# Kernel optimization log

Measured on AMD Instinct MI355X. Metric: run time of the kernel, lower is better.

## Reference

```python
import jax, jax.numpy as jnp
import numpy as np


def setup_inputs() -> dict:
    key = jax.random.key(0)
    k1, k2, k3, k4 = jax.random.split(key, 4)
    Nc, Ng, C = 262144, 393216, 32
    DIM = 96  # N_VOX / 2**(N_LAYER - scale - 1) with scale=2
    return {
        "current_values": jax.random.normal(k1, (Nc, C), dtype=jnp.float32),
        "global_values": jax.random.normal(k2, (Ng, C), dtype=jnp.float32),
        "current_coords": jax.random.randint(k3, (Nc, 3), 0, DIM, dtype=jnp.int32),
        "global_coords": jax.random.randint(k4, (Ng, 3), 0, 110, dtype=jnp.int32),
        "relative_origin": jnp.zeros((3,), dtype=jnp.int32),
        "dim": DIM,
    }


def reference(current_values, global_values, current_coords, global_coords,
              relative_origin, dim):
    """GRUFusion.convert2dense (FUSION.FULL=False) + the gather of the dense
    hidden/input features at the updated (=current) coords that feeds ConvGRU.
    Returns [Nc, 2C]: concat(x_gather, h_gather)."""
    C = current_values.shape[-1]
    cc = current_coords  # [Nc,3], guaranteed in [0, dim)
    gc = global_coords - relative_origin[None, :]  # [Ng,3]

    # in-bounds mask for global coords relative to current fragment bbox
    valid = jnp.all((gc < dim) & (gc >= 0), axis=-1)  # [Ng]

    # occupancy of current coords (sparse_to_dense_torch(current_coords, 1, ...))
    occ = jnp.zeros((dim, dim, dim), jnp.int32)
    occ = occ.at[cc[:, 0], cc[:, 1], cc[:, 2]].set(1)

    # gather occupancy at (clamped-safe) global coords; refine valid mask
    gc_safe = jnp.where(valid[:, None], gc, 0)
    hit = occ[gc_safe[:, 0], gc_safe[:, 1], gc_safe[:, 2]] != 0
    valid = valid & hit

    # sparse_to_dense_channel(global_coords[valid], global_value[valid], ...):
    # route invalid rows out of bounds so the scatter drops them.
    gc_scat = jnp.where(valid[:, None], gc, dim)
    global_vol = jnp.zeros((dim, dim, dim, C), global_values.dtype)
    global_vol = global_vol.at[gc_scat[:, 0], gc_scat[:, 1], gc_scat[:, 2]].set(
        global_values, mode='drop')

    # sparse_to_dense_channel(current_coords, current_values, ...)
    current_vol = jnp.zeros((dim, dim, dim, C), current_values.dtype)
    current_vol = current_vol.at[cc[:, 0], cc[:, 1], cc[:, 2]].set(current_values)

    # updated_coords = current_coords (FUSION.FULL is False); gather GRU inputs
    h = global_vol[cc[:, 0], cc[:, 1], cc[:, 2]]   # hidden state  [Nc,C]
    x = current_vol[cc[:, 0], cc[:, 1], cc[:, 2]]  # current input [Nc,C]
    return jnp.concatenate([x, h], axis=-1)  # [Nc, 2C]
```

## Files before the change

kernel.cpp:

```cpp
#include <hip/hip_runtime.h>

#define DIMC 96
#define VOX (DIMC * DIMC * DIMC)
#define C 32

typedef float f32x4 __attribute__((ext_vector_type(4)));

__global__ void scatter_idx_both(const int* __restrict__ cc,
                                 const int* __restrict__ gc,
                                 const int* __restrict__ origin,
                                 int nc, int ng,
                                 int* __restrict__ cmap,
                                 int* __restrict__ gmap) {
    int i = blockIdx.x * blockDim.x + threadIdx.x;
    if (i < nc) {
        int x = cc[3 * i + 0];
        int y = cc[3 * i + 1];
        int z = cc[3 * i + 2];
        atomicMax(&cmap[(x * DIMC + y) * DIMC + z], i);
    } else {
        int k = i - nc;
        if (k < ng) {
            int x = gc[3 * k + 0] - origin[0];
            int y = gc[3 * k + 1] - origin[1];
            int z = gc[3 * k + 2] - origin[2];
            if ((unsigned)x < (unsigned)DIMC && (unsigned)y < (unsigned)DIMC &&
                (unsigned)z < (unsigned)DIMC) {
                atomicMax(&gmap[(x * DIMC + y) * DIMC + z], k);
            }
        }
    }
}

__global__ void gather_out_kernel(const f32x4* __restrict__ cur_vals,
                                  const f32x4* __restrict__ glob_vals,
                                  const int* __restrict__ cc,
                                  const int* __restrict__ cmap,
                                  const int* __restrict__ gmap,
                                  int nc, f32x4* __restrict__ out) {
    const int lane = threadIdx.x & 15;
    const int sub  = threadIdx.x >> 4;
    const int base = blockIdx.x * 64 + sub;
    const bool isx = lane < 8;
    const int* __restrict__ map = isx ? cmap : gmap;
    const f32x4* __restrict__ src = isx ? cur_vals : glob_vals;
    const int l = lane & 7;

    int p[4], v[4], j[4];
    f32x4 r[4];

#pragma unroll
    for (int q = 0; q < 4; ++q) p[q] = base + q * 16;

#pragma unroll
    for (int q = 0; q < 4; ++q) {
        int pp = p[q] < nc ? p[q] : 0;
        int x = cc[3 * pp + 0];
        int y = cc[3 * pp + 1];
        int z = cc[3 * pp + 2];
        v[q] = (x * DIMC + y) * DIMC + z;
    }
#pragma unroll
    for (int q = 0; q < 4; ++q) j[q] = map[v[q]];
#pragma unroll
    for (int q = 0; q < 4; ++q) {
        r[q] = (f32x4)(0.f);
        if (j[q] >= 0) r[q] = src[(size_t)j[q] * 8 + l];
    }
#pragma unroll
    for (int q = 0; q < 4; ++q) {
        if (p[q] < nc)
            __builtin_nontemporal_store(r[q], &out[(size_t)p[q] * 16 + lane]);
    }
}

extern "C" void kernel_launch(void* const* d_in, const int* in_sizes, int n_in,
                              void* d_out, int out_size, void* d_ws, size_t ws_size,
                              hipStream_t stream) {
    const f32x4* cur_vals = (const f32x4*)d_in[0];
    const f32x4* glob_vals = (const f32x4*)d_in[1];
    const int* cur_coords = (const int*)d_in[2];
    const int* glob_coords = (const int*)d_in[3];
    const int* rel_origin = (const int*)d_in[4];

    int nc = in_sizes[2] / 3;
    int ng = in_sizes[3] / 3;

    int* cmap = (int*)d_ws;
    int* gmap = cmap + VOX;

    hipMemsetAsync(d_ws, 0xFF, (size_t)2 * VOX * sizeof(int), stream);

    const int B = 256;
    int total = nc + ng;
    scatter_idx_both<<<(total + B - 1) / B, B, 0, stream>>>(
        cur_coords, glob_coords, rel_origin, nc, ng, cmap, gmap);

    int blocks = (nc + 63) / 64;
    gather_out_kernel<<<blocks, B, 0, stream>>>(
        cur_vals, glob_vals, cur_coords, cmap, gmap, nc, (f32x4*)d_out);
}
```

Baseline: 167.7 us.

## Vectorize coord loads, cache voxel ids, and double gather work per block

```diff
diff --git a/kernel.cpp b/kernel.cpp
--- a/kernel.cpp
+++ b/kernel.cpp
@@ -6,69 +6,101 @@
 
 typedef float f32x4 __attribute__((ext_vector_type(4)));
 
-__global__ void scatter_idx_both(const int* __restrict__ cc,
+__device__ __forceinline__ int voxid(int x, int y, int z) {
+    return (x * DIMC + y) * DIMC + z;
+}
+
+__global__ void scatter_idx_both(const int4* __restrict__ cc4,
+                                 const int4* __restrict__ gc4,
+                                 const int* __restrict__ cc,
                                  const int* __restrict__ gc,
                                  const int* __restrict__ origin,
                                  int nc, int ng,
                                  int* __restrict__ cmap,
-                                 int* __restrict__ gmap) {
-    int i = blockIdx.x * blockDim.x + threadIdx.x;
-    if (i < nc) {
-        int x = cc[3 * i + 0];
-        int y = cc[3 * i + 1];
-        int z = cc[3 * i + 2];
-        atomicMax(&cmap[(x * DIMC + y) * DIMC + z], i);
-    } else {
-        int k = i - nc;
-        if (k < ng) {
-            int x = gc[3 * k + 0] - origin[0];
-            int y = gc[3 * k + 1] - origin[1];
-            int z = gc[3 * k + 2] - origin[2];
+                                 int* __restrict__ gmap,
+                                 int* __restrict__ cvox) {
+    const int nq_c = nc >> 2, nq_g = ng >> 2;
+    int t = blockIdx.x * blockDim.x + threadIdx.x;
+
+    if (t < nq_c) {
+        int4 a = cc4[3 * t], b = cc4[3 * t + 1], c = cc4[3 * t + 2];
+        int i = 4 * t;
+        int v0 = voxid(a.x, a.y, a.z);
+        int v1 = voxid(a.w, b.x, b.y);
+        int v2 = voxid(b.z, b.w, c.x);
+        int v3 = voxid(c.y, c.z, c.w);
+        atomicMax(&cmap[v0], i);
+        atomicMax(&cmap[v1], i + 1);
+        atomicMax(&cmap[v2], i + 2);
+        atomicMax(&cmap[v3], i + 3);
+        *reinterpret_cast<int4*>(cvox + i) = make_int4(v0, v1, v2, v3);
+    } else if (t - nq_c < nq_g) {
+        int k4 = t - nq_c;
+        int4 a = gc4[3 * k4], b = gc4[3 * k4 + 1], c = gc4[3 * k4 + 2];
+        int ox = origin[0], oy = origin[1], oz = origin[2];
+        int k = 4 * k4;
+        int xs[4] = {a.x - ox, a.w - ox, b.z - ox, c.y - ox};
+        int ys[4] = {a.y - oy, b.x - oy, b.w - oy, c.z - oy};
+        int zs[4] = {a.z - oz, b.y - oz, c.x - oz, c.w - oz};
+#pragma unroll
+        for (int q = 0; q < 4; ++q) {
+            if ((unsigned)xs[q] < (unsigned)DIMC &&
+                (unsigned)ys[q] < (unsigned)DIMC &&
+                (unsigned)zs[q] < (unsigned)DIMC) {
+                atomicMax(&gmap[voxid(xs[q], ys[q], zs[q])], k + q);
+            }
+        }
+    } else if (t == nq_c + nq_g) {
+        for (int i = nq_c * 4; i < nc; ++i) {
+            int v = voxid(cc[3 * i], cc[3 * i + 1], cc[3 * i + 2]);
+            atomicMax(&cmap[v], i);
+            cvox[i] = v;
+        }
+    } else if (t == nq_c + nq_g + 1) {
+        int ox = origin[0], oy = origin[1], oz = origin[2];
+        for (int k = nq_g * 4; k < ng; ++k) {
+            int x = gc[3 * k] - ox, y = gc[3 * k + 1] - oy, z = gc[3 * k + 2] - oz;
             if ((unsigned)x < (unsigned)DIMC && (unsigned)y < (unsigned)DIMC &&
-                (unsigned)z < (unsigned)DIMC) {
-                atomicMax(&gmap[(x * DIMC + y) * DIMC + z], k);
-            }
+                (unsigned)z < (unsigned)DIMC)
+                atomicMax(&gmap[voxid(x, y, z)], k);
         }
     }
 }
 
-__global__ void gather_out_kernel(const f32x4* __restrict__ cur_vals,
-                                  const f32x4* __restrict__ glob_vals,
-                                  const int* __restrict__ cc,
-                                  const int* __restrict__ cmap,
-                                  const int* __restrict__ gmap,
-                                  int nc, f32x4* __restrict__ out) {
+__global__ __launch_bounds__(256) void gather_out_kernel(
+    const f32x4* __restrict__ cur_vals,
+    const f32x4* __restrict__ glob_vals,
+    const int* __restrict__ cvox,
+    const int* __restrict__ cmap,
+    const int* __restrict__ gmap,
+    int nc, f32x4* __restrict__ out) {
     const int lane = threadIdx.x & 15;
-    const int sub  = threadIdx.x >> 4;
-    const int base = blockIdx.x * 64 + sub;
+    const int sub = threadIdx.x >> 4;
+    const int base = blockIdx.x * 128 + sub;
     const bool isx = lane < 8;
     const int* __restrict__ map = isx ? cmap : gmap;
     const f32x4* __restrict__ src = isx ? cur_vals : glob_vals;
     const int l = lane & 7;
 
-    int p[4], v[4], j[4];
-    f32x4 r[4];
+    int p[8], v[8], j[8];
+    f32x4 r[8];
 
 #pragma unroll
-    for (int q = 0; q < 4; ++q) p[q] = base + q * 16;
-
+    for (int q = 0; q < 8; ++q) p[q] = base + q * 16;
 #pragma unroll
-    for (int q = 0; q < 4; ++q) {
+    for (int q = 0; q < 8; ++q) {
         int pp = p[q] < nc ? p[q] : 0;
-        int x = cc[3 * pp + 0];
-        int y = cc[3 * pp + 1];
-        int z = cc[3 * pp + 2];
-        v[q] = (x * DIMC + y) * DIMC + z;
+        v[q] = cvox[pp];
     }
 #pragma unroll
-    for (int q = 0; q < 4; ++q) j[q] = map[v[q]];
+    for (int q = 0; q < 8; ++q) j[q] = map[v[q]];
 #pragma unroll
-    for (int q = 0; q < 4; ++q) {
+    for (int q = 0; q < 8; ++q) {
         r[q] = (f32x4)(0.f);
         if (j[q] >= 0) r[q] = src[(size_t)j[q] * 8 + l];
     }
 #pragma unroll
-    for (int q = 0; q < 4; ++q) {
+    for (int q = 0; q < 8; ++q) {
         if (p[q] < nc)
             __builtin_nontemporal_store(r[q], &out[(size_t)p[q] * 16 + lane]);
     }
@@ -88,15 +120,17 @@
 
     int* cmap = (int*)d_ws;
     int* gmap = cmap + VOX;
+    int* cvox = gmap + VOX;
 
     hipMemsetAsync(d_ws, 0xFF, (size_t)2 * VOX * sizeof(int), stream);
 
     const int B = 256;
-    int total = nc + ng;
-    scatter_idx_both<<<(total + B - 1) / B, B, 0, stream>>>(
-        cur_coords, glob_coords, rel_origin, nc, ng, cmap, gmap);
+    int nthreads = (nc >> 2) + (ng >> 2) + 2;
+    scatter_idx_both<<<(nthreads + B - 1) / B, B, 0, stream>>>(
+        (const int4*)cur_coords, (const int4*)glob_coords,
+        cur_coords, glob_coords, rel_origin, nc, ng, cmap, gmap, cvox);
 
-    int blocks = (nc + 63) / 64;
+    int blocks = (nc + 127) / 128;
     gather_out_kernel<<<blocks, B, 0, stream>>>(
-        cur_vals, glob_vals, cur_coords, cmap, gmap, nc, (f32x4*)d_out);
+        cur_vals, glob_vals, cvox, cmap, gmap, nc, (f32x4*)d_out);
 }
```

Result: slower. 183.5 us (+9.5%).
